# Performance work log

Measured on AMD Instinct MI355X. Metric: run time of the kernel, lower is better.

## Reference

```python
import jax, jax.numpy as jnp
import numpy as np

D, S, E, MPE = 256, 128, 512, 4096
B, N = 2, 4096


def _rope(x):
    # x: (..., n, d); RoPE over axis -2 positions (dim=1 in the torch code)
    n, d = x.shape[-2], x.shape[-1]
    half = d // 2
    pos = jnp.arange(n, dtype=x.dtype)
    inv_freq = 10000.0 ** (-jnp.arange(half, dtype=x.dtype) / half)
    sinusoid = pos[:, None] * inv_freq  # (n, half)
    sin, cos = jnp.sin(sinusoid), jnp.cos(sinusoid)
    x1, x2 = jnp.split(x, 2, axis=-1)
    return jnp.concatenate([x1 * cos - x2 * sin, x2 * cos + x1 * sin], axis=-1)


def setup_inputs() -> dict:
    key = jax.random.key(0)
    ks = jax.random.split(key, 12)
    std = 0.02
    return {
        "query": jax.random.normal(ks[0], (B, N, D), jnp.float32),
        "ln_w": jnp.ones((D,), jnp.float32),
        "ln_b": jnp.zeros((D,), jnp.float32),
        "Wu": jax.random.normal(ks[1], (D, E), jnp.float32) / np.float32(np.sqrt(D)),
        "bu": jnp.zeros((E,), jnp.float32),
        "Wv": jax.random.normal(ks[2], (D, E), jnp.float32) / np.float32(np.sqrt(D)),
        "bv": jnp.zeros((E,), jnp.float32),
        "Wbase": jax.random.normal(ks[3], (D, S), jnp.float32) / np.float32(np.sqrt(D)),
        "bbase": jnp.zeros((S,), jnp.float32),
        "q_w": jax.random.normal(ks[4], (1, S), jnp.float32) * std,
        "q_b": jnp.zeros((1, S), jnp.float32),
        "k_w": jax.random.normal(ks[5], (1, S), jnp.float32) * std,
        "k_b": jnp.zeros((1, S), jnp.float32),
        "w_rel": jax.random.normal(ks[6], (2 * MPE - 1,), jnp.float32) * std,
        "Wo": jax.random.normal(ks[7], (E, D), jnp.float32) / np.float32(np.sqrt(E)),
        "bo": jnp.zeros((D,), jnp.float32),
    }


def reference(query, ln_w, ln_b, Wu, bu, Wv, bv, Wbase, bbase,
              q_w, q_b, k_w, k_b, w_rel, Wo, bo):
    mpe = (w_rel.shape[0] + 1) // 2
    bsz, n, d = query.shape
    # LayerNorm
    mu = query.mean(axis=-1, keepdims=True)
    var = ((query - mu) ** 2).mean(axis=-1, keepdims=True)
    x = (query - mu) * jax.lax.rsqrt(var + 1e-5) * ln_w + ln_b
    # gated projections
    u = jax.nn.silu(x @ Wu + bu)       # (B,N,E)
    v = jax.nn.silu(x @ Wv + bv)       # (B,N,E)
    base = jax.nn.silu(x @ Wbase + bbase)  # (B,N,S)
    q = _rope(base * q_w + q_b)
    k = _rope(base * k_w + k_b)
    qk = jnp.einsum('bms,bns->bmn', q, k)  # (B,N,N)
    # Toeplitz relative-position bias: bias[i,j] = w_rel[mpe-1 + j - i]
    # (equivalent to the torch pad/repeat/reshape construction, sliced to n)
    i = jnp.arange(n)
    bias = w_rel[(mpe - 1) + i[None, :] - i[:, None]]  # (N,N)
    kernel = jnp.square(jax.nn.relu(qk / mpe + bias))
    out = (u * jnp.einsum('bmn,bne->bme', kernel, v)) @ Wo + bo
    return out
```

## Files before the change

kernel.cpp:

```cpp
#include <hip/hip_runtime.h>
#include <hip/hip_bf16.h>
#include <math.h>

typedef __bf16 bf16_8 __attribute__((ext_vector_type(8)));
typedef float f32x4 __attribute__((ext_vector_type(4)));

#define D_ 256
#define S_ 128
#define E_ 512
#define MPE_ 4096
#define B_ 2
#define N_ 4096
#define M_TOT (B_*N_)

__device__ __forceinline__ ushort f2b(float f) {
  union { float f; uint u; } x; x.f = f;
  uint r = (x.u + 0x7FFFu + ((x.u >> 16) & 1u)) >> 16;
  return (ushort)r;
}
__device__ __forceinline__ float b2f(ushort b) {
  union { uint u; float f; } x; x.u = ((uint)b) << 16;
  return x.f;
}

__device__ __forceinline__ void gl_lds16(const void* g, void* l) {
  __builtin_amdgcn_global_load_lds(
      (const __attribute__((address_space(1))) void*)g,
      (__attribute__((address_space(3))) void*)l, 16, 0, 0);
}

__global__ __launch_bounds__(256) void ln_kernel(const float* __restrict__ q,
    const float* __restrict__ w, const float* __restrict__ b,
    ushort* __restrict__ x) {
  int wid = threadIdx.x >> 6, lane = threadIdx.x & 63;
  int row = blockIdx.x * 4 + wid;
  const float* qr = q + (size_t)row * D_;
  float4 v = *(const float4*)(qr + lane * 4);
  float s  = v.x + v.y + v.z + v.w;
  float ss = v.x*v.x + v.y*v.y + v.z*v.z + v.w*v.w;
  #pragma unroll
  for (int off = 32; off; off >>= 1) {
    s  += __shfl_xor(s, off);
    ss += __shfl_xor(ss, off);
  }
  float mu   = s * (1.0f / 256.0f);
  float var  = ss * (1.0f / 256.0f) - mu * mu;
  float rstd = rsqrtf(var + 1e-5f);
  ushort4 o;
  float vv[4] = {v.x, v.y, v.z, v.w};
  ushort ot[4];
  #pragma unroll
  for (int j = 0; j < 4; ++j) {
    int c = lane * 4 + j;
    ot[j] = f2b((vv[j] - mu) * rstd * w[c] + b[c]);
  }
  o.x = ot[0]; o.y = ot[1]; o.z = ot[2]; o.w = ot[3];
  *(ushort4*)(x + (size_t)row * D_ + lane * 4) = o;
}

__global__ __launch_bounds__(256) void prep_kernel(
    const float* __restrict__ Wu, const float* __restrict__ Wv,
    const float* __restrict__ Wb, const float* __restrict__ Wo,
    const float* __restrict__ w_rel,
    ushort* __restrict__ WUT, ushort* __restrict__ WVT,
    ushort* __restrict__ WBT, ushort* __restrict__ WOT,
    float* __restrict__ wrep) {
  int blk = blockIdx.x, tid = threadIdx.x;
  if (blk < 512) {
    int o = blk * 256 + tid; int c = o >> 8, r = o & 255;
    WUT[o] = f2b(Wu[r * 512 + c]);
  } else if (blk < 1024) {
    int o = (blk - 512) * 256 + tid; int c = o >> 8, r = o & 255;
    WVT[o] = f2b(Wv[r * 512 + c]);
  } else if (blk < 1152) {
    int o = (blk - 1024) * 256 + tid; int c = o >> 8, r = o & 255;
    WBT[o] = f2b(Wb[r * 128 + c]);
  } else if (blk < 1664) {
    int o = (blk - 1152) * 256 + tid; int c = o >> 9, r = o & 511;
    WOT[o] = f2b(Wo[r * 256 + c]);
  } else {
    int idx = (blk - 1664) * 256 + tid;
    int c = idx >> 13, i = idx & 8191;
    int s = i + c; if (s > 8190) s = 8190;
    wrep[idx] = w_rel[s];
  }
}

template<int EPI>
__global__ __launch_bounds__(256) void gemm_kernel(
    const ushort* __restrict__ A, const ushort* __restrict__ Bt,
    const float* __restrict__ bias, void* __restrict__ out,
    int M, int N, int K) {
  __shared__ alignas(16) ushort As[128 * 64];
  __shared__ alignas(16) ushort Bs[64 * 64];
  int tid = threadIdx.x;
  int lane = tid & 63, wid = tid >> 6;
  int m0 = blockIdx.x * 128, n0 = blockIdx.y * 64;
  int r16 = lane & 15, kq = lane >> 4;
  f32x4 acc[2][4] = {};
  for (int k0 = 0; k0 < K; k0 += 64) {
    __syncthreads();
    #pragma unroll
    for (int t = 0; t < 4; ++t) {
      int cid = tid + t * 256;
      int row = cid >> 3, c = cid & 7;
      uint4 d = *(const uint4*)(A + ((size_t)(m0 + row) * K + k0 + c * 8));
      *(uint4*)&As[row * 64 + ((c ^ (row & 7)) * 8)] = d;
    }
    #pragma unroll
    for (int t = 0; t < 2; ++t) {
      int cid = tid + t * 256;
      int row = cid >> 3, c = cid & 7;
      uint4 d = *(const uint4*)(Bt + ((size_t)(n0 + row) * K + k0 + c * 8));
      *(uint4*)&Bs[row * 64 + ((c ^ (row & 7)) * 8)] = d;
    }
    __syncthreads();
    #pragma unroll
    for (int ks = 0; ks < 2; ++ks) {
      bf16_8 af[2], bfr[4];
      int c = ks * 4 + kq;
      #pragma unroll
      for (int fm = 0; fm < 2; ++fm) {
        int r = wid * 32 + fm * 16 + r16;
        af[fm] = *(const bf16_8*)&As[r * 64 + ((c ^ (r & 7)) * 8)];
      }
      #pragma unroll
      for (int fn = 0; fn < 4; ++fn) {
        int r = fn * 16 + r16;
        bfr[fn] = *(const bf16_8*)&Bs[r * 64 + ((c ^ (r & 7)) * 8)];
      }
      #pragma unroll
      for (int fm = 0; fm < 2; ++fm)
        #pragma unroll
        for (int fn = 0; fn < 4; ++fn)
          acc[fm][fn] = __builtin_amdgcn_mfma_f32_16x16x32_bf16(af[fm], bfr[fn], acc[fm][fn], 0, 0, 0);
    }
  }
  #pragma unroll
  for (int fm = 0; fm < 2; ++fm)
    #pragma unroll
    for (int fn = 0; fn < 4; ++fn)
      #pragma unroll
      for (int reg = 0; reg < 4; ++reg) {
        int ml = wid * 32 + fm * 16 + kq * 4 + reg;
        int nl = fn * 16 + r16;
        size_t gm = m0 + ml, gn = n0 + nl;
        float val = acc[fm][fn][reg] + bias[gn];
        if (EPI == 0) {
          float y = val / (1.0f + expf(-val));
          ((ushort*)out)[gm * N + gn] = f2b(y);
        } else if (EPI == 2) {
          float y = val / (1.0f + expf(-val));
          ((ushort*)out)[gn * (size_t)M_TOT + gm] = f2b(y);
        } else {
          ((float*)out)[gm * N + gn] = val;
        }
      }
}

__global__ __launch_bounds__(256) void rope_kernel(const ushort* __restrict__ base,
    const float* __restrict__ qw, const float* __restrict__ qb,
    const float* __restrict__ kw, const float* __restrict__ kb,
    ushort* __restrict__ Q, ushort* __restrict__ Kk) {
  int g = blockIdx.x * 256 + threadIdx.x;
  int row = g >> 6, i = g & 63;
  int n = row & (N_ - 1);
  float invf = powf(10000.0f, -(float)i * (1.0f / 64.0f));
  float sv, cv;
  sincosf((float)n * invf, &sv, &cv);
  const float sc = 0.015625f;
  float b1 = b2f(base[row * S_ + i]), b2 = b2f(base[row * S_ + 64 + i]);
  float x1q = b1 * qw[i] + qb[i], x2q = b2 * qw[64 + i] + qb[64 + i];
  Q[row * S_ + i]      = f2b((x1q * cv - x2q * sv) * sc);
  Q[row * S_ + 64 + i] = f2b((x2q * cv + x1q * sv) * sc);
  float x1k = b1 * kw[i] + kb[i], x2k = b2 * kw[64 + i] + kb[64 + i];
  Kk[row * S_ + i]      = f2b((x1k * cv - x2k * sv) * sc);
  Kk[row * S_ + 64 + i] = f2b((x2k * cv + x1k * sv) * sc);
}

__global__ __launch_bounds__(256, 2) void attn_kernel(
    const ushort* __restrict__ Q, const ushort* __restrict__ Kd,
    const ushort* __restrict__ VT, const ushort* __restrict__ U,
    const float* __restrict__ wrep, ushort* __restrict__ KVU) {
  __shared__ alignas(16) ushort Ks[2][64 * 128];
  __shared__ alignas(16) ushort Vs[2][128 * 64];
  __shared__ alignas(16) ushort Pb[64 * 64];
  const int tid = threadIdx.x, lane = tid & 63, wid = tid >> 6;
  const int b = blockIdx.z, m0 = blockIdx.x * 64, e0 = blockIdx.y * 128;
  const int r16 = lane & 15, kq = lane >> 4;
  const int wn = wid;
  const int wpm = wid >> 1, wpe = wid & 1;

  const int bbase = 4095 + 16 * wn + 4 * kq - m0 - r16;
  const int csel = bbase & 3;
  const float* wrow = wrep + csel * 8192 + (bbase - csel);

  bf16_8 qf[4][4];
  #pragma unroll
  for (int fm = 0; fm < 4; ++fm)
    #pragma unroll
    for (int ks = 0; ks < 4; ++ks)
      qf[fm][ks] = *(const bf16_8*)(Q +
          ((size_t)(b * N_ + m0 + fm * 16 + r16) * S_ + ks * 32 + kq * 8));

  auto stage_k = [&](int bi, int nt) {
    int n0s = nt * 64;
    #pragma unroll
    for (int tt = 0; tt < 4; ++tt) {
      int p = tt * 256 + tid;
      int row = p >> 4, sc2 = p & 15;
      int cc = sc2 ^ (row & 7);
      gl_lds16(Kd + ((size_t)(b * N_ + n0s + row) * S_ + cc * 8),
               (char*)&Ks[bi][0] + (tt * 256 + wid * 64) * 16);
    }
  };
  auto stage_v = [&](int bi, int nt) {
    int n0s = nt * 64;
    #pragma unroll
    for (int tt = 0; tt < 4; ++tt) {
      int p = tt * 256 + tid;
      int er = p >> 3, sc2 = p & 7;
      int nc = sc2 ^ (er & 7);
      gl_lds16(VT + ((size_t)(e0 + er) * M_TOT + b * N_ + n0s + nc * 8),
               (char*)&Vs[bi][0] + (tt * 256 + wid * 64) * 16);
    }
  };

  f32x4 pv[2][4] = {};
  const char* psb = (const char*)&Pb[0];

  auto do_pv = [&](int vb) {
    const ushort* vsb = &Vs[vb][0];
    __builtin_amdgcn_s_setprio(1);
    #pragma unroll
    for (int ks = 0; ks < 2; ++ks) {
      bf16_8 pa[2];
      #pragma unroll
      for (int fm = 0; fm < 2; ++fm) {
        int r = wpm * 32 + fm * 16 + r16;
        pa[fm] = *(const bf16_8*)(psb + ((r * 128 + ks * 64 + kq * 16) ^ ((r & 7) << 4)));
      }
      #pragma unroll
      for (int fe = 0; fe < 4; ++fe) {
        int rv = wpe * 64 + fe * 16 + r16;
        int cv = ks * 4 + kq;
        bf16_8 vf = *(const bf16_8*)&vsb[rv * 64 + ((cv ^ (rv & 7)) * 8)];
        #pragma unroll
        for (int fm = 0; fm < 2; ++fm)
          pv[fm][fe] = __builtin_amdgcn_mfma_f32_16x16x32_bf16(pa[fm], vf, pv[fm][fe], 0, 0, 0);
      }
    }
    __builtin_amdgcn_s_setprio(0);
  };

  stage_k(0, 0);
  asm volatile("s_waitcnt vmcnt(0) lgkmcnt(0)" ::: "memory");
  __builtin_amdgcn_s_barrier();

  auto body = [&](int t, int cur, bool doK) {
    float4 b4[4];
    #pragma unroll
    for (int fm = 0; fm < 4; ++fm)
      b4[fm] = *(const float4*)(wrow + 64 * t - 16 * fm);
    if (doK) stage_k(cur ^ 1, t + 1);
    stage_v(cur, t);
    __builtin_amdgcn_sched_barrier(0);
    const ushort* ksb = &Ks[cur][0];
    f32x4 sacc[4] = {};
    __builtin_amdgcn_s_setprio(1);
    #pragma unroll
    for (int ks = 0; ks < 4; ++ks) {
      int r = wn * 16 + r16;
      int c = ks * 4 + kq;
      bf16_8 kf = *(const bf16_8*)&ksb[r * 128 + ((c ^ (r & 7)) * 8)];
      #pragma unroll
      for (int fm = 0; fm < 4; ++fm)
        sacc[fm] = __builtin_amdgcn_mfma_f32_16x16x32_bf16(kf, qf[fm][ks], sacc[fm], 0, 0, 0);
    }
    __builtin_amdgcn_s_setprio(0);
    if (t > 0) do_pv(cur ^ 1);
    asm volatile("s_waitcnt lgkmcnt(0)" ::: "memory");
    __builtin_amdgcn_s_barrier();
    #pragma unroll
    for (int fm = 0; fm < 4; ++fm) {
      float t0 = fmaxf(sacc[fm][0] + b4[fm].x, 0.f); t0 *= t0;
      float t1 = fmaxf(sacc[fm][1] + b4[fm].y, 0.f); t1 *= t1;
      float t2 = fmaxf(sacc[fm][2] + b4[fm].z, 0.f); t2 *= t2;
      float t3 = fmaxf(sacc[fm][3] + b4[fm].w, 0.f); t3 *= t3;
      uint p01, p23;
      asm("v_cvt_pk_bf16_f32 %0, %1, %2" : "=v"(p01) : "v"(t0), "v"(t1));
      asm("v_cvt_pk_bf16_f32 %0, %1, %2" : "=v"(p23) : "v"(t2), "v"(t3));
      int mp = fm * 16 + r16;
      int nb2 = wn * 32 + kq * 8;
      uint2 pk; pk.x = p01; pk.y = p23;
      *(uint2*)((char*)&Pb[0] + ((mp * 128 + nb2) ^ ((mp & 7) << 4))) = pk;
    }
    asm volatile("s_waitcnt vmcnt(0) lgkmcnt(0)" ::: "memory");
    __builtin_amdgcn_s_barrier();
  };

  for (int t2 = 0; t2 < 32; ++t2) {
    body(2 * t2, 0, true);
    body(2 * t2 + 1, 1, 2 * t2 + 1 < 63);
  }
  do_pv(1);

  #pragma unroll
  for (int fm = 0; fm < 2; ++fm)
    #pragma unroll
    for (int fe = 0; fe < 4; ++fe)
      #pragma unroll
      for (int reg = 0; reg < 4; ++reg) {
        int ml = wpm * 32 + fm * 16 + kq * 4 + reg;
        size_t grow = (size_t)b * N_ + m0 + ml;
        size_t ge = e0 + wpe * 64 + fe * 16 + r16;
        float uu = b2f(U[grow * E_ + ge]);
        KVU[grow * E_ + ge] = f2b(uu * pv[fm][fe][reg]);
      }
}

extern "C" void kernel_launch(void* const* d_in, const int* in_sizes, int n_in,
                              void* d_out, int out_size, void* d_ws, size_t ws_size,
                              hipStream_t stream) {
  const float* query = (const float*)d_in[0];
  const float* ln_w  = (const float*)d_in[1];
  const float* ln_b  = (const float*)d_in[2];
  const float* Wu    = (const float*)d_in[3];
  const float* bu    = (const float*)d_in[4];
  const float* Wv    = (const float*)d_in[5];
  const float* bv    = (const float*)d_in[6];
  const float* Wbase = (const float*)d_in[7];
  const float* bbase = (const float*)d_in[8];
  const float* q_w   = (const float*)d_in[9];
  const float* q_b   = (const float*)d_in[10];
  const float* k_w   = (const float*)d_in[11];
  const float* k_b   = (const float*)d_in[12];
  const float* w_rel = (const float*)d_in[13];
  const float* Wo    = (const float*)d_in[14];
  const float* bo    = (const float*)d_in[15];
  float* out = (float*)d_out;

  char* ws = (char*)d_ws;
  ushort* X    = (ushort*)(ws);
  ushort* U    = (ushort*)(ws + (4u  << 20));
  ushort* VT   = (ushort*)(ws + (12u << 20));
  ushort* BASE = (ushort*)(ws + (20u << 20));
  ushort* Qb   = (ushort*)(ws + (22u << 20));
  ushort* Kb   = (ushort*)(ws + (24u << 20));
  ushort* KVU  = (ushort*)(ws + (26u << 20));
  ushort* WUT  = (ushort*)(ws + (34u << 20));
  ushort* WVT  = (ushort*)(ws + (34u << 20) + 512*256*2);
  ushort* WBT  = (ushort*)(ws + (34u << 20) + 2*512*256*2);
  ushort* WOT  = (ushort*)(ws + (34u << 20) + 2*512*256*2 + 128*256*2);
  float*  WREP = (float*)(ws + (35u << 20));

  ln_kernel<<<2048, 256, 0, stream>>>(query, ln_w, ln_b, X);
  prep_kernel<<<1792, 256, 0, stream>>>(Wu, Wv, Wbase, Wo, w_rel,
                                        WUT, WVT, WBT, WOT, WREP);
  gemm_kernel<0><<<dim3(64, 8), 256, 0, stream>>>(X, WUT, bu, U, 8192, 512, 256);
  gemm_kernel<2><<<dim3(64, 8), 256, 0, stream>>>(X, WVT, bv, VT, 8192, 512, 256);
  gemm_kernel<0><<<dim3(64, 2), 256, 0, stream>>>(X, WBT, bbase, BASE, 8192, 128, 256);
  rope_kernel<<<2048, 256, 0, stream>>>(BASE, q_w, q_b, k_w, k_b, Qb, Kb);
  attn_kernel<<<dim3(64, 4, 2), 256, 0, stream>>>(Qb, Kb, VT, U, WREP, KVU);
  gemm_kernel<1><<<dim3(64, 4), 256, 0, stream>>>(KVU, WOT, bo, out, 8192, 256, 512);
}
```

Before: 161.2 us.

## Prepack K and V in MFMA fragment layout and load directly to registers

The producer kernels (rope for K, the V projection epilogue) now write K and V in a pre-swizzled fragment-major layout, so each lane's MFMA operand is one contiguous 16-byte global load. The attention kernel drops the LDS staging buffers for K and V and loads fragments straight into registers. It double-buffers only the P tile in LDS and software-pipelines the K/V register loads across iterations. This removes the LDS traffic and staging overhead but makes each block reload K/V from L2 without sharing, and scatters the producer writes.

Result: slower. 164.6 us (+2.1%).

```diff
diff --git a/kernel.cpp b/kernel.cpp
--- a/kernel.cpp
+++ b/kernel.cpp
@@ -21,12 +21,6 @@
 __device__ __forceinline__ float b2f(ushort b) {
   union { uint u; float f; } x; x.u = ((uint)b) << 16;
   return x.f;
-}
-
-__device__ __forceinline__ void gl_lds16(const void* g, void* l) {
-  __builtin_amdgcn_global_load_lds(
-      (const __attribute__((address_space(1))) void*)g,
-      (__attribute__((address_space(3))) void*)l, 16, 0, 0);
 }
 
 __global__ __launch_bounds__(256) void ln_kernel(const float* __restrict__ q,
@@ -151,7 +145,12 @@
           ((ushort*)out)[gm * N + gn] = f2b(y);
         } else if (EPI == 2) {
           float y = val / (1.0f + expf(-val));
-          ((ushort*)out)[gn * (size_t)M_TOT + gm] = f2b(y);
+          int bb = (int)(gm >> 12), n = (int)(gm & 4095);
+          int t = n >> 6, nn = n & 63;
+          int ks2 = nn >> 5, kq2 = (nn >> 3) & 3, j = nn & 7;
+          size_t addr = ((size_t)((bb * 64 + t) * 2 + ks2) * 32 + (gn >> 4)) * 512
+                      + (kq2 * 16 + (gn & 15)) * 8 + j;
+          ((ushort*)out)[addr] = f2b(y);
         } else {
           ((float*)out)[gm * N + gn] = val;
         }
@@ -161,7 +160,7 @@
 __global__ __launch_bounds__(256) void rope_kernel(const ushort* __restrict__ base,
     const float* __restrict__ qw, const float* __restrict__ qb,
     const float* __restrict__ kw, const float* __restrict__ kb,
-    ushort* __restrict__ Q, ushort* __restrict__ Kk) {
+    ushort* __restrict__ Q, ushort* __restrict__ KF) {
   int g = blockIdx.x * 256 + threadIdx.x;
   int row = g >> 6, i = g & 63;
   int n = row & (N_ - 1);
@@ -174,19 +173,23 @@
   Q[row * S_ + i]      = f2b((x1q * cv - x2q * sv) * sc);
   Q[row * S_ + 64 + i] = f2b((x2q * cv + x1q * sv) * sc);
   float x1k = b1 * kw[i] + kb[i], x2k = b2 * kw[64 + i] + kb[64 + i];
-  Kk[row * S_ + i]      = f2b((x1k * cv - x2k * sv) * sc);
-  Kk[row * S_ + 64 + i] = f2b((x2k * cv + x1k * sv) * sc);
+  float k1 = (x1k * cv - x2k * sv) * sc;
+  float k2 = (x2k * cv + x1k * sv) * sc;
+  int bb = row >> 12, nn = n & 63, t = n >> 6;
+  int wn = nn >> 4, r16 = nn & 15;
+  size_t kbase = ((size_t)((bb * 64 + t) * 16 + wn * 4)) * 512 + r16 * 8;
+  int ks1 = i >> 5, kq1 = (i >> 3) & 3, j = i & 7;
+  KF[kbase + ks1 * 512 + kq1 * 128 + j] = f2b(k1);
+  KF[kbase + (2 + ks1) * 512 + kq1 * 128 + j] = f2b(k2);
 }
 
 __global__ __launch_bounds__(256, 2) void attn_kernel(
-    const ushort* __restrict__ Q, const ushort* __restrict__ Kd,
-    const ushort* __restrict__ VT, const ushort* __restrict__ U,
+    const ushort* __restrict__ Q, const ushort* __restrict__ KF,
+    const ushort* __restrict__ VF, const ushort* __restrict__ U,
     const float* __restrict__ wrep, ushort* __restrict__ KVU) {
-  __shared__ alignas(16) ushort Ks[2][64 * 128];
-  __shared__ alignas(16) ushort Vs[2][128 * 64];
-  __shared__ alignas(16) ushort Pb[64 * 64];
+  __shared__ alignas(16) ushort Pb[2][64 * 64];
   const int tid = threadIdx.x, lane = tid & 63, wid = tid >> 6;
-  const int b = blockIdx.z, m0 = blockIdx.x * 64, e0 = blockIdx.y * 128;
+  const int b = blockIdx.z, m0 = blockIdx.x * 64;
   const int r16 = lane & 15, kq = lane >> 4;
   const int wn = wid;
   const int wpm = wid >> 1, wpe = wid & 1;
@@ -203,34 +206,33 @@
       qf[fm][ks] = *(const bf16_8*)(Q +
           ((size_t)(b * N_ + m0 + fm * 16 + r16) * S_ + ks * 32 + kq * 8));
 
-  auto stage_k = [&](int bi, int nt) {
-    int n0s = nt * 64;
-    #pragma unroll
-    for (int tt = 0; tt < 4; ++tt) {
-      int p = tt * 256 + tid;
-      int row = p >> 4, sc2 = p & 15;
-      int cc = sc2 ^ (row & 7);
-      gl_lds16(Kd + ((size_t)(b * N_ + n0s + row) * S_ + cc * 8),
-               (char*)&Ks[bi][0] + (tt * 256 + wid * 64) * 16);
-    }
-  };
-  auto stage_v = [&](int bi, int nt) {
-    int n0s = nt * 64;
-    #pragma unroll
-    for (int tt = 0; tt < 4; ++tt) {
-      int p = tt * 256 + tid;
-      int er = p >> 3, sc2 = p & 7;
-      int nc = sc2 ^ (er & 7);
-      gl_lds16(VT + ((size_t)(e0 + er) * M_TOT + b * N_ + n0s + nc * 8),
-               (char*)&Vs[bi][0] + (tt * 256 + wid * 64) * 16);
-    }
-  };
-
+  const ushort* kfb = KF + ((size_t)(b * 64) * 16 + wn * 4) * 512 + lane * 8;
+  const ushort* vfb = VF + ((size_t)(b * 64) * 2 * 32 + blockIdx.y * 8 + wpe * 4) * 512 + lane * 8;
+
+  uint4 kf[4], vf[8];
+  float4 b4[4];
   f32x4 pv[2][4] = {};
-  const char* psb = (const char*)&Pb[0];
-
-  auto do_pv = [&](int vb) {
-    const ushort* vsb = &Vs[vb][0];
+
+  auto issue_kf = [&](int t) {
+    #pragma unroll
+    for (int ks = 0; ks < 4; ++ks)
+      kf[ks] = *(const uint4*)(kfb + ((size_t)t * 16 + ks) * 512);
+  };
+  auto issue_vf = [&](int t) {
+    #pragma unroll
+    for (int ks = 0; ks < 2; ++ks)
+      #pragma unroll
+      for (int fe = 0; fe < 4; ++fe)
+        vf[ks * 4 + fe] = *(const uint4*)(vfb + ((size_t)t * 64 + ks * 32 + fe) * 512);
+  };
+  auto issue_bias = [&](int t) {
+    #pragma unroll
+    for (int fm = 0; fm < 4; ++fm)
+      b4[fm] = *(const float4*)(wrow + 64 * t - 16 * fm);
+  };
+
+  auto do_pv = [&](int pi) {
+    const char* psb = (const char*)&Pb[pi][0];
     __builtin_amdgcn_s_setprio(1);
     #pragma unroll
     for (int ks = 0; ks < 2; ++ks) {
@@ -242,45 +244,27 @@
       }
       #pragma unroll
       for (int fe = 0; fe < 4; ++fe) {
-        int rv = wpe * 64 + fe * 16 + r16;
-        int cv = ks * 4 + kq;
-        bf16_8 vf = *(const bf16_8*)&vsb[rv * 64 + ((cv ^ (rv & 7)) * 8)];
+        bf16_8 vfr = *(const bf16_8*)&vf[ks * 4 + fe];
         #pragma unroll
         for (int fm = 0; fm < 2; ++fm)
-          pv[fm][fe] = __builtin_amdgcn_mfma_f32_16x16x32_bf16(pa[fm], vf, pv[fm][fe], 0, 0, 0);
+          pv[fm][fe] = __builtin_amdgcn_mfma_f32_16x16x32_bf16(pa[fm], vfr, pv[fm][fe], 0, 0, 0);
       }
     }
     __builtin_amdgcn_s_setprio(0);
   };
 
-  stage_k(0, 0);
-  asm volatile("s_waitcnt vmcnt(0) lgkmcnt(0)" ::: "memory");
-  __builtin_amdgcn_s_barrier();
-
-  auto body = [&](int t, int cur, bool doK) {
-    float4 b4[4];
-    #pragma unroll
-    for (int fm = 0; fm < 4; ++fm)
-      b4[fm] = *(const float4*)(wrow + 64 * t - 16 * fm);
-    if (doK) stage_k(cur ^ 1, t + 1);
-    stage_v(cur, t);
-    __builtin_amdgcn_sched_barrier(0);
-    const ushort* ksb = &Ks[cur][0];
+  auto qk_transform = [&](int t) {
     f32x4 sacc[4] = {};
     __builtin_amdgcn_s_setprio(1);
     #pragma unroll
     for (int ks = 0; ks < 4; ++ks) {
-      int r = wn * 16 + r16;
-      int c = ks * 4 + kq;
-      bf16_8 kf = *(const bf16_8*)&ksb[r * 128 + ((c ^ (r & 7)) * 8)];
+      bf16_8 kfr = *(const bf16_8*)&kf[ks];
       #pragma unroll
       for (int fm = 0; fm < 4; ++fm)
-        sacc[fm] = __builtin_amdgcn_mfma_f32_16x16x32_bf16(kf, qf[fm][ks], sacc[fm], 0, 0, 0);
+        sacc[fm] = __builtin_amdgcn_mfma_f32_16x16x32_bf16(kfr, qf[fm][ks], sacc[fm], 0, 0, 0);
     }
     __builtin_amdgcn_s_setprio(0);
-    if (t > 0) do_pv(cur ^ 1);
-    asm volatile("s_waitcnt lgkmcnt(0)" ::: "memory");
-    __builtin_amdgcn_s_barrier();
+    char* psb = (char*)&Pb[t & 1][0];
     #pragma unroll
     for (int fm = 0; fm < 4; ++fm) {
       float t0 = fmaxf(sacc[fm][0] + b4[fm].x, 0.f); t0 *= t0;
@@ -293,15 +277,22 @@
       int mp = fm * 16 + r16;
       int nb2 = wn * 32 + kq * 8;
       uint2 pk; pk.x = p01; pk.y = p23;
-      *(uint2*)((char*)&Pb[0] + ((mp * 128 + nb2) ^ ((mp & 7) << 4))) = pk;
-    }
-    asm volatile("s_waitcnt vmcnt(0) lgkmcnt(0)" ::: "memory");
+      *(uint2*)(psb + ((mp * 128 + nb2) ^ ((mp & 7) << 4))) = pk;
+    }
+  };
+
+  issue_kf(0); issue_bias(0); issue_vf(0);
+  qk_transform(0);
+  asm volatile("s_waitcnt lgkmcnt(0)" ::: "memory");
+  __builtin_amdgcn_s_barrier();
+
+  for (int t = 1; t < 64; ++t) {
+    issue_kf(t); issue_bias(t);
+    do_pv((t - 1) & 1);
+    issue_vf(t);
+    qk_transform(t);
+    asm volatile("s_waitcnt lgkmcnt(0)" ::: "memory");
     __builtin_amdgcn_s_barrier();
-  };
-
-  for (int t2 = 0; t2 < 32; ++t2) {
-    body(2 * t2, 0, true);
-    body(2 * t2 + 1, 1, 2 * t2 + 1 < 63);
   }
   do_pv(1);
 
@@ -313,7 +304,7 @@
       for (int reg = 0; reg < 4; ++reg) {
         int ml = wpm * 32 + fm * 16 + kq * 4 + reg;
         size_t grow = (size_t)b * N_ + m0 + ml;
-        size_t ge = e0 + wpe * 64 + fe * 16 + r16;
+        size_t ge = (size_t)blockIdx.y * 128 + wpe * 64 + fe * 16 + r16;
         float uu = b2f(U[grow * E_ + ge]);
         KVU[grow * E_ + ge] = f2b(uu * pv[fm][fe][reg]);
       }
@@ -343,10 +334,10 @@
   char* ws = (char*)d_ws;
   ushort* X    = (ushort*)(ws);
   ushort* U    = (ushort*)(ws + (4u  << 20));
-  ushort* VT   = (ushort*)(ws + (12u << 20));
+  ushort* VF   = (ushort*)(ws + (12u << 20));
   ushort* BASE = (ushort*)(ws + (20u << 20));
   ushort* Qb   = (ushort*)(ws + (22u << 20));
-  ushort* Kb   = (ushort*)(ws + (24u << 20));
+  ushort* KF   = (ushort*)(ws + (24u << 20));
   ushort* KVU  = (ushort*)(ws + (26u << 20));
   ushort* WUT  = (ushort*)(ws + (34u << 20));
   ushort* WVT  = (ushort*)(ws + (34u << 20) + 512*256*2);
@@ -358,9 +349,9 @@
   prep_kernel<<<1792, 256, 0, stream>>>(Wu, Wv, Wbase, Wo, w_rel,
                                         WUT, WVT, WBT, WOT, WREP);
   gemm_kernel<0><<<dim3(64, 8), 256, 0, stream>>>(X, WUT, bu, U, 8192, 512, 256);
-  gemm_kernel<2><<<dim3(64, 8), 256, 0, stream>>>(X, WVT, bv, VT, 8192, 512, 256);
+  gemm_kernel<2><<<dim3(64, 8), 256, 0, stream>>>(X, WVT, bv, VF, 8192, 512, 256);
   gemm_kernel<0><<<dim3(64, 2), 256, 0, stream>>>(X, WBT, bbase, BASE, 8192, 128, 256);
-  rope_kernel<<<2048, 256, 0, stream>>>(BASE, q_w, q_b, k_w, k_b, Qb, Kb);
-  attn_kernel<<<dim3(64, 4, 2), 256, 0, stream>>>(Qb, Kb, VT, U, WREP, KVU);
+  rope_kernel<<<2048, 256, 0, stream>>>(BASE, q_w, q_b, k_w, k_b, Qb, KF);
+  attn_kernel<<<dim3(64, 4, 2), 256, 0, stream>>>(Qb, KF, VF, U, WREP, KVU);
   gemm_kernel<1><<<dim3(64, 4), 256, 0, stream>>>(KVU, WOT, bo, out, 8192, 256, 512);
 }
```

## Enlarge attention tile to 128 query rows with 512 threads and double-buffered P

Applied to the files above, without the earlier changes.

The attention kernel now handles 128 query rows per block with 8 waves instead of 64 rows with 4, so every K/V tile staged into LDS is reused by twice as many rows. This halves the grid size and the per-block global staging traffic. The P buffer is double-buffered, the PV step is moved after a barrier, and the waits are changed to partial vmcnt counts to overlap loads with compute. In exchange, LDS use per block goes up, fewer blocks may fit on each CU, and the hand-tuned vmcnt counts are fragile.

After: 177.3 us. +10.0%, slower.

```diff
diff --git a/kernel.cpp b/kernel.cpp
--- a/kernel.cpp
+++ b/kernel.cpp
@@ -178,20 +178,20 @@
   Kk[row * S_ + 64 + i] = f2b((x2k * cv + x1k * sv) * sc);
 }
 
-__global__ __launch_bounds__(256, 2) void attn_kernel(
+__global__ __launch_bounds__(512, 2) void attn_kernel(
     const ushort* __restrict__ Q, const ushort* __restrict__ Kd,
     const ushort* __restrict__ VT, const ushort* __restrict__ U,
     const float* __restrict__ wrep, ushort* __restrict__ KVU) {
   __shared__ alignas(16) ushort Ks[2][64 * 128];
   __shared__ alignas(16) ushort Vs[2][128 * 64];
-  __shared__ alignas(16) ushort Pb[64 * 64];
+  __shared__ alignas(16) ushort Pb[2][128 * 64];
   const int tid = threadIdx.x, lane = tid & 63, wid = tid >> 6;
-  const int b = blockIdx.z, m0 = blockIdx.x * 64, e0 = blockIdx.y * 128;
+  const int b = blockIdx.z, m0 = blockIdx.x * 128, e0 = blockIdx.y * 128;
   const int r16 = lane & 15, kq = lane >> 4;
-  const int wn = wid;
+  const int wqm = wid >> 2, wqn = wid & 3;
   const int wpm = wid >> 1, wpe = wid & 1;
 
-  const int bbase = 4095 + 16 * wn + 4 * kq - m0 - r16;
+  const int bbase = 4095 + 16 * wqn + 4 * kq - m0 - 64 * wqm - r16;
   const int csel = bbase & 3;
   const float* wrow = wrep + csel * 8192 + (bbase - csel);
 
@@ -201,36 +201,36 @@
     #pragma unroll
     for (int ks = 0; ks < 4; ++ks)
       qf[fm][ks] = *(const bf16_8*)(Q +
-          ((size_t)(b * N_ + m0 + fm * 16 + r16) * S_ + ks * 32 + kq * 8));
+          ((size_t)(b * N_ + m0 + wqm * 64 + fm * 16 + r16) * S_ + ks * 32 + kq * 8));
 
   auto stage_k = [&](int bi, int nt) {
     int n0s = nt * 64;
     #pragma unroll
-    for (int tt = 0; tt < 4; ++tt) {
-      int p = tt * 256 + tid;
+    for (int tt = 0; tt < 2; ++tt) {
+      int p = tt * 512 + tid;
       int row = p >> 4, sc2 = p & 15;
       int cc = sc2 ^ (row & 7);
       gl_lds16(Kd + ((size_t)(b * N_ + n0s + row) * S_ + cc * 8),
-               (char*)&Ks[bi][0] + (tt * 256 + wid * 64) * 16);
+               &Ks[bi][(tt * 512 + wid * 64) * 8]);
     }
   };
   auto stage_v = [&](int bi, int nt) {
     int n0s = nt * 64;
     #pragma unroll
-    for (int tt = 0; tt < 4; ++tt) {
-      int p = tt * 256 + tid;
+    for (int tt = 0; tt < 2; ++tt) {
+      int p = tt * 512 + tid;
       int er = p >> 3, sc2 = p & 7;
       int nc = sc2 ^ (er & 7);
       gl_lds16(VT + ((size_t)(e0 + er) * M_TOT + b * N_ + n0s + nc * 8),
-               (char*)&Vs[bi][0] + (tt * 256 + wid * 64) * 16);
+               &Vs[bi][(tt * 512 + wid * 64) * 8]);
     }
   };
 
   f32x4 pv[2][4] = {};
-  const char* psb = (const char*)&Pb[0];
-
-  auto do_pv = [&](int vb) {
-    const ushort* vsb = &Vs[vb][0];
+
+  auto do_pv = [&](int pi) {
+    const char* psb = (const char*)&Pb[pi][0];
+    const ushort* vsb = &Vs[pi][0];
     __builtin_amdgcn_s_setprio(1);
     #pragma unroll
     for (int ks = 0; ks < 2; ++ks) {
@@ -257,20 +257,20 @@
   asm volatile("s_waitcnt vmcnt(0) lgkmcnt(0)" ::: "memory");
   __builtin_amdgcn_s_barrier();
 
-  auto body = [&](int t, int cur, bool doK) {
+  auto body = [&](int CUR, int t) {
     float4 b4[4];
     #pragma unroll
     for (int fm = 0; fm < 4; ++fm)
       b4[fm] = *(const float4*)(wrow + 64 * t - 16 * fm);
-    if (doK) stage_k(cur ^ 1, t + 1);
-    stage_v(cur, t);
+    if (t < 63) stage_k(CUR ^ 1, t + 1);
+    stage_v(CUR, t);
     __builtin_amdgcn_sched_barrier(0);
-    const ushort* ksb = &Ks[cur][0];
+    const ushort* ksb = &Ks[CUR][0];
     f32x4 sacc[4] = {};
     __builtin_amdgcn_s_setprio(1);
     #pragma unroll
     for (int ks = 0; ks < 4; ++ks) {
-      int r = wn * 16 + r16;
+      int r = wqn * 16 + r16;
       int c = ks * 4 + kq;
       bf16_8 kf = *(const bf16_8*)&ksb[r * 128 + ((c ^ (r & 7)) * 8)];
       #pragma unroll
@@ -278,9 +278,11 @@
         sacc[fm] = __builtin_amdgcn_mfma_f32_16x16x32_bf16(kf, qf[fm][ks], sacc[fm], 0, 0, 0);
     }
     __builtin_amdgcn_s_setprio(0);
-    if (t > 0) do_pv(cur ^ 1);
-    asm volatile("s_waitcnt lgkmcnt(0)" ::: "memory");
+    asm volatile("s_waitcnt vmcnt(8)" ::: "memory");
     __builtin_amdgcn_s_barrier();
+    if (t > 0) do_pv(CUR ^ 1);
+    __builtin_amdgcn_s_barrier();
+    char* psb = (char*)&Pb[CUR][0];
     #pragma unroll
     for (int fm = 0; fm < 4; ++fm) {
       float t0 = fmaxf(sacc[fm][0] + b4[fm].x, 0.f); t0 *= t0;
@@ -290,19 +292,22 @@
       uint p01, p23;
       asm("v_cvt_pk_bf16_f32 %0, %1, %2" : "=v"(p01) : "v"(t0), "v"(t1));
       asm("v_cvt_pk_bf16_f32 %0, %1, %2" : "=v"(p23) : "v"(t2), "v"(t3));
-      int mp = fm * 16 + r16;
-      int nb2 = wn * 32 + kq * 8;
+      int mp = wqm * 64 + fm * 16 + r16;
+      int nb2 = wqn * 32 + kq * 8;
       uint2 pk; pk.x = p01; pk.y = p23;
-      *(uint2*)((char*)&Pb[0] + ((mp * 128 + nb2) ^ ((mp & 7) << 4))) = pk;
-    }
-    asm volatile("s_waitcnt vmcnt(0) lgkmcnt(0)" ::: "memory");
+      *(uint2*)(psb + ((mp * 128 + nb2) ^ ((mp & 7) << 4))) = pk;
+    }
+    asm volatile("s_waitcnt lgkmcnt(0)" ::: "memory");
+    asm volatile("s_waitcnt vmcnt(2)" ::: "memory");
     __builtin_amdgcn_s_barrier();
   };
 
   for (int t2 = 0; t2 < 32; ++t2) {
-    body(2 * t2, 0, true);
-    body(2 * t2 + 1, 1, 2 * t2 + 1 < 63);
-  }
+    body(0, 2 * t2);
+    body(1, 2 * t2 + 1);
+  }
+  asm volatile("s_waitcnt vmcnt(0)" ::: "memory");
+  __builtin_amdgcn_s_barrier();
   do_pv(1);
 
   #pragma unroll
@@ -361,6 +366,6 @@
   gemm_kernel<2><<<dim3(64, 8), 256, 0, stream>>>(X, WVT, bv, VT, 8192, 512, 256);
   gemm_kernel<0><<<dim3(64, 2), 256, 0, stream>>>(X, WBT, bbase, BASE, 8192, 128, 256);
   rope_kernel<<<2048, 256, 0, stream>>>(BASE, q_w, q_b, k_w, k_b, Qb, Kb);
-  attn_kernel<<<dim3(64, 4, 2), 256, 0, stream>>>(Qb, Kb, VT, U, WREP, KVU);
+  attn_kernel<<<dim3(32, 4, 2), 512, 0, stream>>>(Qb, Kb, VT, U, WREP, KVU);
   gemm_kernel<1><<<dim3(64, 4), 256, 0, stream>>>(KVU, WOT, bo, out, 8192, 256, 512);
 }
```
